# Kernel optimization log

Hardware: AMD Instinct MI355X
Metric: run time of the kernel (lower is better)

The kernel has to match this reference:

```python
import jax, jax.numpy as jnp
import numpy as np

N, E, ND, ED, H, L = 50000, 800000, 64, 32, 128, 4
MIN = 2 * H + H + 1  # message MLP input dim = 385
EPS = 1e-5


def _layernorm(x, w, b):
    mu = x.mean(-1, keepdims=True)
    var = ((x - mu) ** 2).mean(-1, keepdims=True)
    return (x - mu) / jnp.sqrt(var + EPS) * w + b


def setup_inputs() -> dict:
    key = jax.random.key(0)
    ks = jax.random.split(key, 40)

    def w(k, shape):
        return jax.random.normal(k, shape, jnp.float32) / np.sqrt(shape[-2]).astype(np.float32)

    inp = {
        "node_features": jax.random.normal(ks[0], (N, ND), jnp.float32),
        "edge_features": jax.random.normal(ks[1], (E, ED), jnp.float32),
        "congestion": jax.random.uniform(ks[2], (N,), jnp.float32),
        "edge_index": jax.random.randint(ks[3], (2, E), 0, N),
        "unrouted_mask": jax.random.randint(ks[4], (N,), 0, 2).astype(jnp.bool_),
        "enc_node_w": w(ks[5], (ND, H)), "enc_node_b": jnp.zeros(H),
        "enc_edge_w": w(ks[6], (ED, H)), "enc_edge_b": jnp.zeros(H),
        "msg_w1": w(ks[7], (L, MIN, H)), "msg_b1": jnp.zeros((L, H)),
        "msg_w2": w(ks[8], (L, H, H)), "msg_b2": jnp.zeros((L, H)),
        "upd_w1": w(ks[9], (L, 2 * H, H)), "upd_b1": jnp.zeros((L, H)),
        "upd_w2": w(ks[10], (L, H, H)), "upd_b2": jnp.zeros((L, H)),
        "ln_w": jnp.ones((L, H)), "ln_b": jnp.zeros((L, H)),
        "unr_w1": w(ks[11], (1, H)), "unr_b1": jnp.zeros(H),
        "unr_w2": w(ks[12], (H, H)), "unr_b2": jnp.zeros(H),
        "ro_w1": w(ks[13], (2 * H, H)), "ro_b1": jnp.zeros(H),
        "ro_w2": w(ks[14], (H, H // 2)), "ro_b2": jnp.zeros(H // 2),
        "ro_w3": w(ks[15], (H // 2, 1)), "ro_b3": jnp.zeros(1),
    }
    return inp


def reference(node_features, edge_features, congestion, edge_index, unrouted_mask,
              enc_node_w, enc_node_b, enc_edge_w, enc_edge_b,
              msg_w1, msg_b1, msg_w2, msg_b2,
              upd_w1, upd_b1, upd_w2, upd_b2,
              ln_w, ln_b,
              unr_w1, unr_b1, unr_w2, unr_b2,
              ro_w1, ro_b1, ro_w2, ro_b2, ro_w3, ro_b3):
    n = node_features.shape[0]
    src, dst = edge_index[0], edge_index[1]

    x = node_features @ enc_node_w + enc_node_b            # [N, H]
    ea = edge_features @ enc_edge_w + enc_edge_b           # [E, H]
    cong_src = congestion[src][:, None]                    # [E, 1]

    for l in range(msg_w1.shape[0]):
        # message: gather src/dst features, concat with edge attr + congestion
        m_in = jnp.concatenate([x[src], x[dst], ea, cong_src], axis=-1)  # [E, 385]
        m = jax.nn.relu(m_in @ msg_w1[l] + msg_b1[l]) @ msg_w2[l] + msg_b2[l]  # [E, H]
        agg = jax.ops.segment_sum(m, dst, num_segments=n)  # scatter_add over dst
        u_in = jnp.concatenate([x, agg], axis=-1)          # [N, 2H]
        x_new = jax.nn.relu(u_in @ upd_w1[l] + upd_b1[l]) @ upd_w2[l] + upd_b2[l]
        x = _layernorm(x + x_new, ln_w[l], ln_b[l])        # dropout = identity (eval)

    graph_embed = x.mean(axis=0, keepdims=True)            # [1, H] (batch=None branch)
    unrouted_frac = unrouted_mask.astype(jnp.float32).mean()[None, None]  # [1, 1]
    unr = jax.nn.relu(unrouted_frac @ unr_w1 + unr_b1) @ unr_w2 + unr_b2  # [1, H]
    combined = jnp.concatenate([graph_embed, unr], axis=-1)  # [1, 2H]
    h = jax.nn.relu(combined @ ro_w1 + ro_b1)
    h = jax.nn.relu(h @ ro_w2 + ro_b2)
    out = jax.nn.sigmoid(h @ ro_w3 + ro_b3)                # [1, 1]
    return out.squeeze(-1)                                 # [1]
```

## Files before the change

kernel.cpp:

```cpp
#include <hip/hip_runtime.h>
#include <hip/hip_fp16.h>
#include <math.h>

#define NN 50000
#define EE 800000

typedef _Float16 half8 __attribute__((ext_vector_type(8)));
typedef __fp16 fp16x2 __attribute__((ext_vector_type(2)));
typedef float floatx4 __attribute__((ext_vector_type(4)));

__global__ void fold_kernel(const float* __restrict__ ew, const float* __restrict__ eb,
                            const float* __restrict__ w1, const float* __restrict__ b1,
                            float* __restrict__ Wc, float* __restrict__ b1f) {
  int l = blockIdx.y, c = blockIdx.x, j = threadIdx.x;
  __shared__ float row[128];
  const float* w1l = w1 + (size_t)l * 385 * 128;
  if (c < 32) {
    row[j] = ew[c * 128 + j];
    __syncthreads();
    float acc = 0.f;
    for (int k = 0; k < 128; k++) acc += row[k] * w1l[(256 + k) * 128 + j];
    Wc[((size_t)l * 32 + c) * 128 + j] = acc;
  } else {
    row[j] = eb[j];
    __syncthreads();
    float acc = b1[l * 128 + j];
    for (int k = 0; k < 128; k++) acc += row[k] * w1l[(256 + k) * 128 + j];
    b1f[l * 128 + j] = acc;
  }
}

__global__ void prep_w(const float* __restrict__ src, _Float16* __restrict__ dst,
                       int K, int perm) {
  int l = blockIdx.y;
  int lane = threadIdx.x;
  int kc = blockIdx.x >> 3, nt = blockIdx.x & 7;
  int n = nt * 16 + (lane & 15);
  int k0 = kc * 32 + (lane >> 4) * 8;
  const float* s = src + (size_t)l * K * 128;
  _Float16 out[8];
  for (int j = 0; j < 8; j++) {
    int k = k0 + j;
    int ks = perm ? ((k & 7) * 16 + (k >> 3)) : k;
    out[j] = (_Float16)s[(size_t)ks * 128 + n];
  }
  _Float16* d = dst + (((size_t)l * gridDim.x + blockIdx.x) * 64 + lane) * 8;
  *(half8*)d = *(half8*)out;
}

__global__ void prep_cong(const float* __restrict__ mw1, _Float16* __restrict__ w1cp) {
  int l = blockIdx.x, p = threadIdx.x;
  int col = (p & 7) * 16 + (p >> 3);
  w1cp[l * 128 + p] = (_Float16)mw1[((size_t)l * 385 + 384) * 128 + col];
}

__global__ void hist_kernel(const int* __restrict__ dstv, int* __restrict__ counts) {
  int e = blockIdx.x * 256 + threadIdx.x;
  if (e < EE) atomicAdd(&counts[dstv[e]], 1);
}

__global__ void scan1_kernel(const int* __restrict__ counts, int* __restrict__ offs,
                             int* __restrict__ bsum) {
  __shared__ int ws[16];
  int t = threadIdx.x, lane = t & 63, w = t >> 6;
  int i = blockIdx.x * 1024 + t;
  int v = (i < NN) ? counts[i] : 0;
  int s = v;
  for (int off = 1; off < 64; off <<= 1) {
    int u = __shfl_up(s, off);
    if (lane >= off) s += u;
  }
  if (lane == 63) ws[w] = s;
  __syncthreads();
  if (w == 0) {
    int u = (lane < 16) ? ws[lane] : 0;
    for (int off = 1; off < 16; off <<= 1) {
      int x = __shfl_up(u, off);
      if (lane >= off && lane < 16) u += x;
    }
    if (lane < 16) ws[lane] = u;
  }
  __syncthreads();
  int wbase = (w > 0) ? ws[w - 1] : 0;
  if (i < NN) offs[i] = wbase + s - v;
  if (t == 0) bsum[blockIdx.x] = ws[15];
}

__global__ void scan2_kernel(int* __restrict__ bsum) {
  int t = threadIdx.x;
  int v = (t < 49) ? bsum[t] : 0;
  int s = v;
  for (int off = 1; off < 64; off <<= 1) {
    int u = __shfl_up(s, off);
    if (t >= off) s += u;
  }
  if (t < 49) bsum[t] = s - v;
}

__global__ void slot1_kernel(const int* __restrict__ dstv, const int* __restrict__ offs,
                             const int* __restrict__ bsum, int* __restrict__ cursor,
                             int* __restrict__ einv) {
  int e = blockIdx.x * 256 + threadIdx.x;
  if (e >= EE) return;
  int d = dstv[e];
  int p = offs[d] + bsum[d >> 10] + atomicAdd(&cursor[d], 1);
  einv[p] = e;
}

__global__ void slot2_kernel(const int* __restrict__ einv, const int* __restrict__ srcv,
                             const int* __restrict__ dstv, const float* __restrict__ ef,
                             int2* __restrict__ meta, _Float16* __restrict__ efh) {
  int p = blockIdx.x * 256 + threadIdx.x;
  if (p >= EE) return;
  int e = einv[p];
  int2 m;
  m.x = srcv[e];
  m.y = dstv[e];
  meta[p] = m;
  const float* sp = ef + (size_t)e * 32;
  _Float16* dp = efh + (size_t)p * 32;
  for (int i = 0; i < 4; i++) {
    float4 f = *(const float4*)(sp + i * 8);
    float4 g = *(const float4*)(sp + i * 8 + 4);
    half8 v;
    v[0] = (_Float16)f.x; v[1] = (_Float16)f.y; v[2] = (_Float16)f.z; v[3] = (_Float16)f.w;
    v[4] = (_Float16)g.x; v[5] = (_Float16)g.y; v[6] = (_Float16)g.z; v[7] = (_Float16)g.w;
    *(half8*)(dp + i * 8) = v;
  }
}

__global__ void enc_mfma(const float* __restrict__ nf, const _Float16* __restrict__ Wenc,
                         const float* __restrict__ bn, _Float16* __restrict__ xh) {
  int t = threadIdx.x, wave = t >> 6, lane = t & 63;
  int quad = lane >> 4, l15 = lane & 15;
  long nb0 = (long)blockIdx.x * 64 + wave * 16;
  long rn = nb0 + l15;
  if (rn >= NN) rn = NN - 1;

  floatx4 acc[8] = {};
  for (int kc = 0; kc < 2; kc++) {
    const float* p = nf + rn * 64 + kc * 32 + quad * 8;
    float4 f0 = *(const float4*)p;
    float4 f1 = *(const float4*)(p + 4);
    half8 a;
    a[0] = (_Float16)f0.x; a[1] = (_Float16)f0.y;
    a[2] = (_Float16)f0.z; a[3] = (_Float16)f0.w;
    a[4] = (_Float16)f1.x; a[5] = (_Float16)f1.y;
    a[6] = (_Float16)f1.z; a[7] = (_Float16)f1.w;
    const _Float16* bp = Wenc + (size_t)(kc * 8) * 512 + lane * 8;
    for (int nt = 0; nt < 8; nt++) {
      half8 b = *(const half8*)(bp + nt * 512);
      acc[nt] = __builtin_amdgcn_mfma_f32_16x16x32_f16(a, b, acc[nt], 0, 0, 0);
    }
  }
  float bv[8];
  for (int nt = 0; nt < 8; nt++) bv[nt] = bn[nt * 16 + l15];
  for (int reg = 0; reg < 4; reg++) {
    long n = nb0 + quad * 4 + reg;
    if (n < NN) {
      for (int nt = 0; nt < 8; nt++)
        xh[n * 128 + nt * 16 + l15] = (_Float16)(acc[nt][reg] + bv[nt]);
    }
  }
}

__global__ __launch_bounds__(256, 3) void sd_kernel(
    const _Float16* __restrict__ xh, const _Float16* __restrict__ WSa,
    const _Float16* __restrict__ WSb, const float* __restrict__ b1f,
    _Float16* __restrict__ Sh, _Float16* __restrict__ Dh) {
  int t = threadIdx.x, wave = t >> 6, lane = t & 63;
  int quad = lane >> 4, l15 = lane & 15;
  long nb0 = (long)blockIdx.x * 64 + wave * 16;
  long rn = nb0 + l15;
  if (rn >= NN) rn = NN - 1;

  floatx4 as_[8] = {}, ad[8] = {};
#pragma unroll
  for (int kc = 0; kc < 4; kc++) {
    half8 a = *(const half8*)(xh + rn * 128 + kc * 32 + quad * 8);
    const _Float16* bpa = WSa + (size_t)(kc * 8) * 512 + lane * 8;
    const _Float16* bpb = WSb + (size_t)(kc * 8) * 512 + lane * 8;
#pragma unroll
    for (int nt = 0; nt < 8; nt++) {
      half8 ba = *(const half8*)(bpa + nt * 512);
      half8 bb = *(const half8*)(bpb + nt * 512);
      as_[nt] = __builtin_amdgcn_mfma_f32_16x16x32_f16(a, ba, as_[nt], 0, 0, 0);
      ad[nt] = __builtin_amdgcn_mfma_f32_16x16x32_f16(a, bb, ad[nt], 0, 0, 0);
    }
  }
  float bbv[8];
  for (int nt = 0; nt < 8; nt++) bbv[nt] = b1f[nt * 16 + l15];
  for (int reg = 0; reg < 4; reg++) {
    long n = nb0 + quad * 4 + reg;
    if (n < NN) {
      half8 hs, hd;
      for (int nt = 0; nt < 8; nt++) {
        hs[nt] = (_Float16)as_[nt][reg];
        hd[nt] = (_Float16)(ad[nt][reg] + bbv[nt]);
      }
      *(half8*)(Sh + n * 128 + l15 * 8) = hs;
      *(half8*)(Dh + n * 128 + l15 * 8) = hd;
    }
  }
}

__global__ __launch_bounds__(256, 4) void msg_kernel(
    const _Float16* __restrict__ Sh, const _Float16* __restrict__ Dh,
    const _Float16* __restrict__ efh, const int2* __restrict__ meta,
    const float* __restrict__ cong,
    const _Float16* __restrict__ Wcp, const _Float16* __restrict__ Wp2,
    const _Float16* __restrict__ w1cp, const float* __restrict__ b2,
    __half* __restrict__ agg) {
  __shared__ __align__(16) _Float16 As[128][136];
  __shared__ int s_src[128], s_dst[128];
  __shared__ float s_cg[128];
  int t = threadIdx.x, wave = t >> 6, lane = t & 63;
  int quad = lane >> 4, l15 = lane & 15;

  int orig = blockIdx.x, nwg = gridDim.x;
  int qq = nwg >> 3, rr = nwg & 7;
  int xcd = orig & 7, rk = orig >> 3;
  int bb = (xcd < rr) ? (xcd * (qq + 1) + rk)
                      : (rr * (qq + 1) + (xcd - rr) * qq + rk);
  long eb0 = (long)bb * 128;
  int web = wave * 32;

  if (t < 128) {
    int2 m = meta[eb0 + t];
    s_src[t] = m.x;
    s_dst[t] = m.y;
    s_cg[t] = cong[m.x];
  }
  half8 wcl = *(const half8*)(w1cp + l15 * 8);
  half8 av0 = *(const half8*)(efh + (size_t)(eb0 + web + l15) * 32 + quad * 8);
  half8 av1 = *(const half8*)(efh + (size_t)(eb0 + web + 16 + l15) * 32 + quad * 8);
  __syncthreads();

  half8 sv[8], dv[8];
#pragma unroll
  for (int mtl = 0; mtl < 2; mtl++)
#pragma unroll
    for (int reg = 0; reg < 4; reg++) {
      int r = web + mtl * 16 + quad * 4 + reg;
      sv[mtl * 4 + reg] = *(const half8*)(Sh + (size_t)s_src[r] * 128 + l15 * 8);
      dv[mtl * 4 + reg] = *(const half8*)(Dh + (size_t)s_dst[r] * 128 + l15 * 8);
    }

#pragma unroll
  for (int mtl = 0; mtl < 2; mtl++) {
    half8 a = mtl ? av1 : av0;
    floatx4 e[8] = {};
#pragma unroll
    for (int nt = 0; nt < 8; nt++) {
      half8 b = *(const half8*)(Wcp + (size_t)nt * 512 + lane * 8);
      e[nt] = __builtin_amdgcn_mfma_f32_16x16x32_f16(a, b, e[nt], 0, 0, 0);
    }
#pragma unroll
    for (int reg = 0; reg < 4; reg++) {
      int r = web + mtl * 16 + quad * 4 + reg;
      _Float16 cgh = (_Float16)s_cg[r];
      half8 v = sv[mtl * 4 + reg] + dv[mtl * 4 + reg];
      half8 e8;
#pragma unroll
      for (int i = 0; i < 4; i++) {
        fp16x2 p = __builtin_amdgcn_cvt_pkrtz(e[2 * i][reg], e[2 * i + 1][reg]);
        e8[2 * i] = (_Float16)p[0];
        e8[2 * i + 1] = (_Float16)p[1];
      }
      v += e8;
      v += wcl * cgh;
#pragma unroll
      for (int i = 0; i < 8; i++) v[i] = v[i] > (_Float16)0 ? v[i] : (_Float16)0;
      *(half8*)&As[r][l15 * 8] = v;
    }
  }
  __syncthreads();

  int nb = wave * 2;
  floatx4 acc2[8][2] = {};
  __builtin_amdgcn_s_setprio(1);
#pragma unroll
  for (int kc = 0; kc < 4; kc++) {
    const _Float16* bp = Wp2 + ((size_t)(kc * 8 + nb)) * 512 + lane * 8;
    half8 b0 = *(const half8*)bp;
    half8 b1v = *(const half8*)(bp + 512);
#pragma unroll
    for (int mt = 0; mt < 8; mt++) {
      half8 a = *(const half8*)&As[mt * 16 + l15][kc * 32 + quad * 8];
      acc2[mt][0] = __builtin_amdgcn_mfma_f32_16x16x32_f16(a, b0, acc2[mt][0], 0, 0, 0);
      acc2[mt][1] = __builtin_amdgcn_mfma_f32_16x16x32_f16(a, b1v, acc2[mt][1], 0, 0, 0);
    }
  }
  __builtin_amdgcn_s_setprio(0);
  __syncthreads();

  {
    float c0 = b2[nb * 16 + l15], c1 = b2[(nb + 1) * 16 + l15];
#pragma unroll
    for (int mt = 0; mt < 8; mt++)
#pragma unroll
      for (int reg = 0; reg < 4; reg++) {
        int row = mt * 16 + quad * 4 + reg;
        As[row][nb * 16 + l15] = (_Float16)(acc2[mt][0][reg] + c0);
        As[row][(nb + 1) * 16 + l15] = (_Float16)(acc2[mt][1][reg] + c1);
      }
  }
  __syncthreads();

  {
    int cp = t & 63;
    int q8 = t >> 6;
    int r0 = q8 * 32;
    __half2 vals[32];
#pragma unroll
    for (int i = 0; i < 32; i++) vals[i] = *(__half2*)&As[r0 + i][cp * 2];
    int cur = s_dst[r0];
    __half2 acc = __float2half2_rn(0.f);
    for (int i = 0; i < 32; i++) {
      int d = s_dst[r0 + i];
      if (d != cur) {
        unsafeAtomicAdd((__half2*)(agg + (long)cur * 128 + cp * 2), acc);
        acc = __float2half2_rn(0.f);
        cur = d;
      }
      acc = __hadd2(acc, vals[i]);
    }
    unsafeAtomicAdd((__half2*)(agg + (long)cur * 128 + cp * 2), acc);
  }
}

__global__ __launch_bounds__(256, 3) void upd_kernel(
    _Float16* __restrict__ xh, const _Float16* __restrict__ agg,
    const _Float16* __restrict__ Wp1, const _Float16* __restrict__ Wp2,
    const float* __restrict__ b1, const float* __restrict__ b2,
    const float* __restrict__ g, const float* __restrict__ bb) {
  __shared__ __align__(16) _Float16 hs[4][16][136];
  int t = threadIdx.x, wave = t >> 6, lane = t & 63;
  int quad = lane >> 4, l15 = lane & 15;
  long nb0 = (long)blockIdx.x * 64 + wave * 16;

  floatx4 acc[8] = {};
  {
    long n = nb0 + l15;
    long rn = n < NN ? n : NN - 1;
    for (int kc = 0; kc < 8; kc++) {
      half8 a;
      if (kc < 4) {
        a = *(const half8*)(xh + rn * 128 + kc * 32 + quad * 8);
      } else {
        a = *(const half8*)(agg + rn * 128 + (kc - 4) * 32 + quad * 8);
      }
      const _Float16* bp = Wp1 + (size_t)(kc * 8) * 512 + lane * 8;
      for (int nt = 0; nt < 8; nt++) {
        half8 b = *(const half8*)(bp + nt * 512);
        acc[nt] = __builtin_amdgcn_mfma_f32_16x16x32_f16(a, b, acc[nt], 0, 0, 0);
      }
    }
  }

  float bbv[8];
  for (int nt = 0; nt < 8; nt++) bbv[nt] = b1[nt * 16 + l15];
  for (int reg = 0; reg < 4; reg++) {
    half8 hv;
    for (int nt = 0; nt < 8; nt++)
      hv[nt] = (_Float16)fmaxf(acc[nt][reg] + bbv[nt], 0.f);
    *(half8*)&hs[wave][quad * 4 + reg][l15 * 8] = hv;
  }
  __syncthreads();

  floatx4 acc2[8] = {};
  for (int kc = 0; kc < 4; kc++) {
    half8 a = *(const half8*)&hs[wave][l15][kc * 32 + quad * 8];
    const _Float16* bp = Wp2 + (size_t)(kc * 8) * 512 + lane * 8;
    for (int nt = 0; nt < 8; nt++) {
      half8 b = *(const half8*)(bp + nt * 512);
      acc2[nt] = __builtin_amdgcn_mfma_f32_16x16x32_f16(a, b, acc2[nt], 0, 0, 0);
    }
  }

  float b2v[8], gv[8], bv[8];
  for (int nt = 0; nt < 8; nt++) {
    int col = nt * 16 + l15;
    b2v[nt] = b2[col]; gv[nt] = g[col]; bv[nt] = bb[col];
  }
  for (int reg = 0; reg < 4; reg++) {
    long n = nb0 + quad * 4 + reg;
    bool ok = n < NN;
    long rn = ok ? n : NN - 1;
    float y[8];
    float s = 0.f;
    for (int nt = 0; nt < 8; nt++) {
      y[nt] = (float)xh[rn * 128 + nt * 16 + l15] + acc2[nt][reg] + b2v[nt];
      s += y[nt];
    }
    s += __shfl_xor(s, 1); s += __shfl_xor(s, 2);
    s += __shfl_xor(s, 4); s += __shfl_xor(s, 8);
    float mu = s * (1.f / 128.f);
    float q = 0.f;
    for (int nt = 0; nt < 8; nt++) {
      y[nt] -= mu;
      q += y[nt] * y[nt];
    }
    q += __shfl_xor(q, 1); q += __shfl_xor(q, 2);
    q += __shfl_xor(q, 4); q += __shfl_xor(q, 8);
    float rstd = rsqrtf(q * (1.f / 128.f) + 1e-5f);
    if (ok) {
      for (int nt = 0; nt < 8; nt++) {
        float o = y[nt] * rstd * gv[nt] + bv[nt];
        xh[n * 128 + nt * 16 + l15] = (_Float16)o;
      }
    }
  }
}

__global__ void reduce_kernel(const _Float16* __restrict__ xh,
                              const int* __restrict__ umask, float* __restrict__ red) {
  int t = threadIdx.x;
  long base = (long)blockIdx.x * 196;
  int j = t & 127, half = t >> 7;
  float acc = 0.f;
  for (int i = 0; i < 98; i++) {
    long n = base + half + 2L * i;
    if (n < NN) acc += (float)xh[n * 128 + j];
  }
  __shared__ float sr[2][128];
  __shared__ float sm[4];
  sr[half][j] = acc;
  float mv = 0.f;
  {
    long n = base + t;
    if (t < 196 && n < NN) mv = (float)umask[n];
  }
  for (int off = 32; off; off >>= 1) mv += __shfl_xor(mv, off);
  if ((t & 63) == 0) sm[t >> 6] = mv;
  __syncthreads();
  if (t < 128) atomicAdd(&red[t], sr[0][t] + sr[1][t]);
  if (t == 0) atomicAdd(&red[128], sm[0] + sm[1] + sm[2] + sm[3]);
}

__global__ void readout_kernel(const float* __restrict__ red,
                               const float* __restrict__ xw1, const float* __restrict__ xb1,
                               const float* __restrict__ xw2, const float* __restrict__ xb2,
                               const float* __restrict__ rw1, const float* __restrict__ rb1,
                               const float* __restrict__ rw2, const float* __restrict__ rb2,
                               const float* __restrict__ rw3, const float* __restrict__ rb3,
                               float* __restrict__ out) {
  __shared__ float sa[128], sb[128], sc[128];
  int j = threadIdx.x;
  const float inv = 1.f / (float)NN;
  float ge = red[j] * inv;
  float uf = red[128] * inv;
  float u1 = fmaxf(uf * xw1[j] + xb1[j], 0.f);
  sa[j] = u1;
  sb[j] = ge;
  __syncthreads();
  float u2 = xb2[j];
  for (int k = 0; k < 128; k++) u2 += sa[k] * xw2[k * 128 + j];
  sc[j] = u2;
  __syncthreads();
  float h1 = rb1[j];
  for (int k = 0; k < 128; k++) h1 += sb[k] * rw1[k * 128 + j];
  for (int k = 0; k < 128; k++) h1 += sc[k] * rw1[(128 + k) * 128 + j];
  h1 = fmaxf(h1, 0.f);
  __syncthreads();
  sa[j] = h1;
  __syncthreads();
  float h2 = 0.f;
  if (j < 64) {
    h2 = rb2[j];
    for (int k = 0; k < 128; k++) h2 += sa[k] * rw2[k * 64 + j];
    h2 = fmaxf(h2, 0.f);
  }
  __syncthreads();
  if (j < 64) sb[j] = h2;
  __syncthreads();
  if (j == 0) {
    float a = rb3[0];
    for (int k = 0; k < 64; k++) a += sb[k] * rw3[k];
    out[0] = 1.f / (1.f + expf(-a));
  }
}

extern "C" void kernel_launch(void* const* d_in, const int* in_sizes, int n_in,
                              void* d_out, int out_size, void* d_ws, size_t ws_size,
                              hipStream_t stream) {
  const float* nf   = (const float*)d_in[0];
  const float* ef   = (const float*)d_in[1];
  const float* cong = (const float*)d_in[2];
  const int*   eidx = (const int*)d_in[3];
  const int*   um   = (const int*)d_in[4];
  const float* enw  = (const float*)d_in[5];
  const float* enb  = (const float*)d_in[6];
  const float* eew  = (const float*)d_in[7];
  const float* eeb  = (const float*)d_in[8];
  const float* mw1  = (const float*)d_in[9];
  const float* mb1  = (const float*)d_in[10];
  const float* mw2  = (const float*)d_in[11];
  const float* mb2  = (const float*)d_in[12];
  const float* uw1  = (const float*)d_in[13];
  const float* ub1  = (const float*)d_in[14];
  const float* uw2  = (const float*)d_in[15];
  const float* ub2  = (const float*)d_in[16];
  const float* lnw  = (const float*)d_in[17];
  const float* lnb  = (const float*)d_in[18];
  const float* xw1  = (const float*)d_in[19];
  const float* xb1  = (const float*)d_in[20];
  const float* xw2  = (const float*)d_in[21];
  const float* xb2  = (const float*)d_in[22];
  const float* rw1  = (const float*)d_in[23];
  const float* rb1  = (const float*)d_in[24];
  const float* rw2  = (const float*)d_in[25];
  const float* rb2  = (const float*)d_in[26];
  const float* rw3  = (const float*)d_in[27];
  const float* rb3  = (const float*)d_in[28];
  float* out = (float*)d_out;

  char* W = (char*)d_ws;
  _Float16* xh    = (_Float16*)(W + 0);
  __half*   agg   = (__half*)(W + 12800000);
  _Float16* efh   = (_Float16*)(W + 25600000);
  _Float16* Sh    = (_Float16*)(W + 76800000);
  _Float16* Dh    = (_Float16*)(W + 89600000);
  int2*     meta  = (int2*)(W + 102400000);
  int*      einv  = (int*)(W + 108800000);
  int*      counts= (int*)(W + 112000000);
  int*      cursor= (int*)(W + 112200000);
  int*      offs  = (int*)(W + 112400000);
  _Float16* WSa   = (_Float16*)(W + 112600000);
  _Float16* WSb   = (_Float16*)(W + 112731072);
  _Float16* Wcp   = (_Float16*)(W + 112862144);
  _Float16* Wm2   = (_Float16*)(W + 112894912);
  _Float16* Wu1   = (_Float16*)(W + 113025984);
  _Float16* Wu2   = (_Float16*)(W + 113288128);
  _Float16* Wen   = (_Float16*)(W + 113419200);
  float*    Wc    = (float*)(W + 113435584);
  float*    b1f   = (float*)(W + 113501120);
  _Float16* w1cp  = (_Float16*)(W + 113503168);
  float*    red   = (float*)(W + 113504192);
  int*      bsum  = (int*)red;

  const int* srcv = eidx;
  const int* dstv = eidx + EE;

  (void)hipMemsetAsync(counts, 0, 400000, stream);
  hist_kernel<<<3125, 256, 0, stream>>>(dstv, counts);
  scan1_kernel<<<49, 1024, 0, stream>>>(counts, offs, bsum);
  scan2_kernel<<<1, 64, 0, stream>>>(bsum);
  slot1_kernel<<<3125, 256, 0, stream>>>(dstv, offs, bsum, cursor, einv);
  slot2_kernel<<<3125, 256, 0, stream>>>(einv, srcv, dstv, ef, meta, efh);

  fold_kernel<<<dim3(33, 4), 128, 0, stream>>>(eew, eeb, mw1, mb1, Wc, b1f);
  prep_w<<<dim3(8, 4), 64, 0, stream>>>(Wc, Wcp, 32, 0);
  prep_w<<<dim3(32, 4), 64, 0, stream>>>(mw1, WSa, 385, 0);
  prep_w<<<dim3(32, 4), 64, 0, stream>>>(mw1 + 128 * 128, WSb, 385, 0);
  prep_w<<<dim3(32, 4), 64, 0, stream>>>(mw2, Wm2, 128, 1);
  prep_w<<<dim3(64, 4), 64, 0, stream>>>(uw1, Wu1, 256, 0);
  prep_w<<<dim3(32, 4), 64, 0, stream>>>(uw2, Wu2, 128, 1);
  prep_w<<<dim3(16, 1), 64, 0, stream>>>(enw, Wen, 64, 0);
  prep_cong<<<4, 128, 0, stream>>>(mw1, w1cp);
  enc_mfma<<<782, 256, 0, stream>>>(nf, Wen, enb, xh);

  for (int l = 0; l < 4; l++) {
    sd_kernel<<<782, 256, 0, stream>>>(
        xh, WSa + (size_t)l * 32 * 512, WSb + (size_t)l * 32 * 512,
        b1f + l * 128, Sh, Dh);
    (void)hipMemsetAsync(agg, 0, (size_t)NN * 128 * sizeof(__half), stream);
    msg_kernel<<<6250, 256, 0, stream>>>(
        Sh, Dh, efh, meta, cong,
        Wcp + (size_t)l * 8 * 512, Wm2 + (size_t)l * 32 * 512,
        w1cp + l * 128, mb2 + l * 128, agg);
    upd_kernel<<<782, 256, 0, stream>>>(
        xh, (const _Float16*)agg,
        Wu1 + (size_t)l * 64 * 512, Wu2 + (size_t)l * 32 * 512,
        ub1 + l * 128, ub2 + l * 128, lnw + l * 128, lnb + l * 128);
  }

  (void)hipMemsetAsync(red, 0, 129 * sizeof(float), stream);
  reduce_kernel<<<256, 256, 0, stream>>>(xh, um, red);
  readout_kernel<<<1, 128, 0, stream>>>(red, xw1, xb1, xw2, xb2,
                                        rw1, rb1, rw2, rb2, rw3, rb3, out);
}
```

Before: 935.9 us.

## Fuse src/dst projection into encoder and update kernels; drop XCD block remap

Removes the separate sd_kernel. The source and destination projections are now computed inside enc_mfma for layer 0 and inside upd_kernel for the next layer, reading the freshly computed rows from shared memory. This saves one launch per layer and one re-read of xh from global memory. It also removes the XCD-aware block index remapping in msg_kernel and uses plain blockIdx, which may change L2 locality. Both fused kernels now hold more registers, which may lower occupancy.

```diff
diff --git a/kernel.cpp b/kernel.cpp
--- a/kernel.cpp
+++ b/kernel.cpp
@@ -130,7 +130,11 @@
 }
 
 __global__ void enc_mfma(const float* __restrict__ nf, const _Float16* __restrict__ Wenc,
-                         const float* __restrict__ bn, _Float16* __restrict__ xh) {
+                         const float* __restrict__ bn, _Float16* __restrict__ xh,
+                         const _Float16* __restrict__ WSa, const _Float16* __restrict__ WSb,
+                         const float* __restrict__ b1f,
+                         _Float16* __restrict__ Sh, _Float16* __restrict__ Dh) {
+  __shared__ __align__(16) _Float16 hs[4][16][136];
   int t = threadIdx.x, wave = t >> 6, lane = t & 63;
   int quad = lane >> 4, l15 = lane & 15;
   long nb0 = (long)blockIdx.x * 64 + wave * 16;
@@ -157,49 +161,42 @@
   for (int nt = 0; nt < 8; nt++) bv[nt] = bn[nt * 16 + l15];
   for (int reg = 0; reg < 4; reg++) {
     long n = nb0 + quad * 4 + reg;
-    if (n < NN) {
-      for (int nt = 0; nt < 8; nt++)
-        xh[n * 128 + nt * 16 + l15] = (_Float16)(acc[nt][reg] + bv[nt]);
-    }
-  }
-}
-
-__global__ __launch_bounds__(256, 3) void sd_kernel(
-    const _Float16* __restrict__ xh, const _Float16* __restrict__ WSa,
-    const _Float16* __restrict__ WSb, const float* __restrict__ b1f,
-    _Float16* __restrict__ Sh, _Float16* __restrict__ Dh) {
-  int t = threadIdx.x, wave = t >> 6, lane = t & 63;
-  int quad = lane >> 4, l15 = lane & 15;
-  long nb0 = (long)blockIdx.x * 64 + wave * 16;
-  long rn = nb0 + l15;
-  if (rn >= NN) rn = NN - 1;
-
-  floatx4 as_[8] = {}, ad[8] = {};
-#pragma unroll
-  for (int kc = 0; kc < 4; kc++) {
-    half8 a = *(const half8*)(xh + rn * 128 + kc * 32 + quad * 8);
-    const _Float16* bpa = WSa + (size_t)(kc * 8) * 512 + lane * 8;
-    const _Float16* bpb = WSb + (size_t)(kc * 8) * 512 + lane * 8;
-#pragma unroll
+    bool ok = n < NN;
     for (int nt = 0; nt < 8; nt++) {
-      half8 ba = *(const half8*)(bpa + nt * 512);
-      half8 bb = *(const half8*)(bpb + nt * 512);
-      as_[nt] = __builtin_amdgcn_mfma_f32_16x16x32_f16(a, ba, as_[nt], 0, 0, 0);
-      ad[nt] = __builtin_amdgcn_mfma_f32_16x16x32_f16(a, bb, ad[nt], 0, 0, 0);
-    }
-  }
-  float bbv[8];
-  for (int nt = 0; nt < 8; nt++) bbv[nt] = b1f[nt * 16 + l15];
-  for (int reg = 0; reg < 4; reg++) {
-    long n = nb0 + quad * 4 + reg;
-    if (n < NN) {
-      half8 hs, hd;
+      _Float16 v = (_Float16)(acc[nt][reg] + bv[nt]);
+      if (ok) xh[n * 128 + nt * 16 + l15] = v;
+      hs[wave][quad * 4 + reg][nt * 16 + l15] = v;
+    }
+  }
+
+  {
+    floatx4 as_[8] = {}, ad[8] = {};
+#pragma unroll
+    for (int kc = 0; kc < 4; kc++) {
+      half8 a = *(const half8*)&hs[wave][l15][kc * 32 + quad * 8];
+      const _Float16* bpa = WSa + (size_t)(kc * 8) * 512 + lane * 8;
+      const _Float16* bpb = WSb + (size_t)(kc * 8) * 512 + lane * 8;
+#pragma unroll
       for (int nt = 0; nt < 8; nt++) {
-        hs[nt] = (_Float16)as_[nt][reg];
-        hd[nt] = (_Float16)(ad[nt][reg] + bbv[nt]);
-      }
-      *(half8*)(Sh + n * 128 + l15 * 8) = hs;
-      *(half8*)(Dh + n * 128 + l15 * 8) = hd;
+        half8 ba = *(const half8*)(bpa + nt * 512);
+        half8 bbq = *(const half8*)(bpb + nt * 512);
+        as_[nt] = __builtin_amdgcn_mfma_f32_16x16x32_f16(a, ba, as_[nt], 0, 0, 0);
+        ad[nt] = __builtin_amdgcn_mfma_f32_16x16x32_f16(a, bbq, ad[nt], 0, 0, 0);
+      }
+    }
+    float bfv[8];
+    for (int nt = 0; nt < 8; nt++) bfv[nt] = b1f[nt * 16 + l15];
+    for (int reg = 0; reg < 4; reg++) {
+      long n = nb0 + quad * 4 + reg;
+      if (n < NN) {
+        half8 hsv, hdv;
+        for (int nt = 0; nt < 8; nt++) {
+          hsv[nt] = (_Float16)as_[nt][reg];
+          hdv[nt] = (_Float16)(ad[nt][reg] + bfv[nt]);
+        }
+        *(half8*)(Sh + n * 128 + l15 * 8) = hsv;
+        *(half8*)(Dh + n * 128 + l15 * 8) = hdv;
+      }
     }
   }
 }
@@ -216,13 +213,7 @@
   __shared__ float s_cg[128];
   int t = threadIdx.x, wave = t >> 6, lane = t & 63;
   int quad = lane >> 4, l15 = lane & 15;
-
-  int orig = blockIdx.x, nwg = gridDim.x;
-  int qq = nwg >> 3, rr = nwg & 7;
-  int xcd = orig & 7, rk = orig >> 3;
-  int bb = (xcd < rr) ? (xcd * (qq + 1) + rk)
-                      : (rr * (qq + 1) + (xcd - rr) * qq + rk);
-  long eb0 = (long)bb * 128;
+  long eb0 = (long)blockIdx.x * 128;
   int web = wave * 32;
 
   if (t < 128) {
@@ -333,7 +324,10 @@
     _Float16* __restrict__ xh, const _Float16* __restrict__ agg,
     const _Float16* __restrict__ Wp1, const _Float16* __restrict__ Wp2,
     const float* __restrict__ b1, const float* __restrict__ b2,
-    const float* __restrict__ g, const float* __restrict__ bb) {
+    const float* __restrict__ g, const float* __restrict__ bb,
+    const _Float16* __restrict__ WSa, const _Float16* __restrict__ WSb,
+    const float* __restrict__ b1f,
+    _Float16* __restrict__ Sh, _Float16* __restrict__ Dh) {
   __shared__ __align__(16) _Float16 hs[4][16][136];
   int t = threadIdx.x, wave = t >> 6, lane = t & 63;
   int quad = lane >> 4, l15 = lane & 15;
@@ -383,6 +377,7 @@
     int col = nt * 16 + l15;
     b2v[nt] = b2[col]; gv[nt] = g[col]; bv[nt] = bb[col];
   }
+  bool fuse = (WSa != nullptr);
   for (int reg = 0; reg < 4; reg++) {
     long n = nb0 + quad * 4 + reg;
     bool ok = n < NN;
@@ -404,10 +399,40 @@
     q += __shfl_xor(q, 1); q += __shfl_xor(q, 2);
     q += __shfl_xor(q, 4); q += __shfl_xor(q, 8);
     float rstd = rsqrtf(q * (1.f / 128.f) + 1e-5f);
-    if (ok) {
+    for (int nt = 0; nt < 8; nt++) {
+      _Float16 o = (_Float16)(y[nt] * rstd * gv[nt] + bv[nt]);
+      if (ok) xh[n * 128 + nt * 16 + l15] = o;
+      if (fuse) hs[wave][quad * 4 + reg][nt * 16 + l15] = o;
+    }
+  }
+
+  if (fuse) {
+    floatx4 as_[8] = {}, ad[8] = {};
+#pragma unroll
+    for (int kc = 0; kc < 4; kc++) {
+      half8 a = *(const half8*)&hs[wave][l15][kc * 32 + quad * 8];
+      const _Float16* bpa = WSa + (size_t)(kc * 8) * 512 + lane * 8;
+      const _Float16* bpb = WSb + (size_t)(kc * 8) * 512 + lane * 8;
+#pragma unroll
       for (int nt = 0; nt < 8; nt++) {
-        float o = y[nt] * rstd * gv[nt] + bv[nt];
-        xh[n * 128 + nt * 16 + l15] = (_Float16)o;
+        half8 ba = *(const half8*)(bpa + nt * 512);
+        half8 bbq = *(const half8*)(bpb + nt * 512);
+        as_[nt] = __builtin_amdgcn_mfma_f32_16x16x32_f16(a, ba, as_[nt], 0, 0, 0);
+        ad[nt] = __builtin_amdgcn_mfma_f32_16x16x32_f16(a, bbq, ad[nt], 0, 0, 0);
+      }
+    }
+    float bfv[8];
+    for (int nt = 0; nt < 8; nt++) bfv[nt] = b1f[nt * 16 + l15];
+    for (int reg = 0; reg < 4; reg++) {
+      long n = nb0 + quad * 4 + reg;
+      if (n < NN) {
+        half8 hsv, hdv;
+        for (int nt = 0; nt < 8; nt++) {
+          hsv[nt] = (_Float16)as_[nt][reg];
+          hdv[nt] = (_Float16)(ad[nt][reg] + bfv[nt]);
+        }
+        *(half8*)(Sh + n * 128 + l15 * 8) = hsv;
+        *(half8*)(Dh + n * 128 + l15 * 8) = hdv;
       }
     }
   }
@@ -558,21 +583,23 @@
   prep_w<<<dim3(32, 4), 64, 0, stream>>>(uw2, Wu2, 128, 1);
   prep_w<<<dim3(16, 1), 64, 0, stream>>>(enw, Wen, 64, 0);
   prep_cong<<<4, 128, 0, stream>>>(mw1, w1cp);
-  enc_mfma<<<782, 256, 0, stream>>>(nf, Wen, enb, xh);
+  enc_mfma<<<782, 256, 0, stream>>>(nf, Wen, enb, xh, WSa, WSb, b1f, Sh, Dh);
 
   for (int l = 0; l < 4; l++) {
-    sd_kernel<<<782, 256, 0, stream>>>(
-        xh, WSa + (size_t)l * 32 * 512, WSb + (size_t)l * 32 * 512,
-        b1f + l * 128, Sh, Dh);
     (void)hipMemsetAsync(agg, 0, (size_t)NN * 128 * sizeof(__half), stream);
     msg_kernel<<<6250, 256, 0, stream>>>(
         Sh, Dh, efh, meta, cong,
         Wcp + (size_t)l * 8 * 512, Wm2 + (size_t)l * 32 * 512,
         w1cp + l * 128, mb2 + l * 128, agg);
+    bool fuse = (l < 3);
     upd_kernel<<<782, 256, 0, stream>>>(
         xh, (const _Float16*)agg,
         Wu1 + (size_t)l * 64 * 512, Wu2 + (size_t)l * 32 * 512,
-        ub1 + l * 128, ub2 + l * 128, lnw + l * 128, lnb + l * 128);
+        ub1 + l * 128, ub2 + l * 128, lnw + l * 128, lnb + l * 128,
+        fuse ? WSa + (size_t)(l + 1) * 32 * 512 : (const _Float16*)nullptr,
+        fuse ? WSb + (size_t)(l + 1) * 32 * 512 : (const _Float16*)nullptr,
+        fuse ? b1f + (l + 1) * 128 : (const float*)nullptr,
+        Sh, Dh);
   }
 
   (void)hipMemsetAsync(red, 0, 129 * sizeof(float), stream);
```

New measurement: 912.5 us. -2.5%, faster.
